# Optimization experiments

Measured on AMD Instinct MI355X. Metric: run time of the kernel, lower is better.

## Reference

```python
import jax, jax.numpy as jnp
import numpy as np
from jax import lax

EPS = 1e-5
T, N, E = 10, 10000, 320000
C_IN, C_HID, C_OUT = 16, 32, 16


def _stgcn_layer(x, edge_index, edge_weight, tw, tb, gw, gb, gamma, beta):
    # x: [T, N, Cin] -> temporal conv over T per node
    xc = jnp.transpose(x, (1, 2, 0))  # [N, Cin, T]
    y = lax.conv_general_dilated(xc, tw, window_strides=(1,), padding=((1, 1),),
                                 dimension_numbers=("NCH", "OIH", "NCH"))
    y = y + tb[None, :, None]
    y = jnp.clip(y, -10.0, 10.0)
    # InstanceNorm1d (affine, biased var over time axis)
    mu = jnp.mean(y, axis=-1, keepdims=True)
    var = jnp.mean((y - mu) ** 2, axis=-1, keepdims=True)
    y = (y - mu) * lax.rsqrt(var + EPS) * gamma[None, :, None] + beta[None, :, None]
    y = jax.nn.relu(y)
    h = jnp.transpose(y, (0, 2, 1))  # [N, T, C]

    n = h.shape[0]
    # GCNConv normalization (identical at every timestep -> computed once)
    ewn = jax.nn.softmax(edge_weight)  # softmax over all E edges
    loop = jnp.arange(n, dtype=edge_index.dtype)
    row = jnp.concatenate([edge_index[0], loop])  # sources (+self loops)
    col = jnp.concatenate([edge_index[1], loop])  # destinations
    w = jnp.concatenate([ewn, jnp.ones((n,), dtype=ewn.dtype)])
    deg = jax.ops.segment_sum(w, col, num_segments=n)
    dinv = jnp.where(deg > 0, lax.rsqrt(jnp.maximum(deg, EPS * 0 + 1e-30)), 0.0)
    norm = dinv[row] * w * dinv[col]  # [E+N]

    hw = jnp.einsum("ntc,cd->ntd", h, gw)  # [N, T, C]
    msg = hw[row] * norm[:, None, None]     # [E+N, T, C] gather
    agg = jax.ops.segment_sum(msg, col, num_segments=n) + gb  # scatter-add
    out = jnp.clip(jax.nn.relu(agg), -10.0, 10.0)
    return jnp.transpose(out, (1, 0, 2))  # [T, N, C]


def setup_inputs() -> dict:
    key = jax.random.key(0)
    ks = jax.random.split(key, 16)
    inp = {
        "x": jax.random.normal(ks[0], (T, N, C_IN), dtype=jnp.float32),
        "edge_index": jax.random.randint(ks[1], (2, E), 0, N, dtype=jnp.int32),
        "edge_weight": jax.random.uniform(ks[2], (E,), dtype=jnp.float32),
        # layer 1 (in -> hid)
        "l1_tw": jax.random.normal(ks[3], (C_HID, C_IN, 3), dtype=jnp.float32) * 0.02,
        "l1_tb": jnp.zeros((C_HID,), dtype=jnp.float32),
        "l1_gw": jax.random.normal(ks[4], (C_HID, C_HID), dtype=jnp.float32) * 0.1,
        "l1_gb": jnp.zeros((C_HID,), dtype=jnp.float32),
        "l1_gamma": jnp.ones((C_HID,), dtype=jnp.float32),
        "l1_beta": jnp.zeros((C_HID,), dtype=jnp.float32),
        # layer 2 (hid -> hid)
        "l2_tw": jax.random.normal(ks[5], (C_HID, C_HID, 3), dtype=jnp.float32) * 0.02,
        "l2_tb": jnp.zeros((C_HID,), dtype=jnp.float32),
        "l2_gw": jax.random.normal(ks[6], (C_HID, C_HID), dtype=jnp.float32) * 0.1,
        "l2_gb": jnp.zeros((C_HID,), dtype=jnp.float32),
        "l2_gamma": jnp.ones((C_HID,), dtype=jnp.float32),
        "l2_beta": jnp.zeros((C_HID,), dtype=jnp.float32),
        # output linear
        "out_w": jax.random.normal(ks[7], (C_HID, C_OUT), dtype=jnp.float32) * 0.1,
        "out_b": jnp.zeros((C_OUT,), dtype=jnp.float32),
    }
    return inp


def reference(x, edge_index, edge_weight,
              l1_tw, l1_tb, l1_gw, l1_gb, l1_gamma, l1_beta,
              l2_tw, l2_tb, l2_gw, l2_gb, l2_gamma, l2_beta,
              out_w, out_b):
    h = _stgcn_layer(x, edge_index, edge_weight, l1_tw, l1_tb, l1_gw, l1_gb, l1_gamma, l1_beta)
    h = _stgcn_layer(h, edge_index, edge_weight, l2_tw, l2_tb, l2_gw, l2_gb, l2_gamma, l2_beta)
    # per-timestep linear then mean over time == mean then linear, done faithfully
    outs = jnp.einsum("tnc,cd->tnd", h, out_w) + out_b
    return jnp.mean(outs, axis=0)  # [N, C_OUT]
```

## Files before the change

kernel.cpp:

```cpp
#include <hip/hip_runtime.h>
#include <hip/hip_bf16.h>
#include <string.h>


typedef __hip_bfloat16 bf16;

#define TSTEPS 10
#define TPAD 12
#define CHID 32
#define ROWELE (TSTEPS * CHID)
#define ROWW4 40

__device__ __forceinline__ float b2f(bf16 v) { return __bfloat162float(v); }
__device__ __forceinline__ float ldf(const void* p, long i, int bf) {
    return bf ? __bfloat162float(((const bf16*)p)[i]) : ((const float*)p)[i];
}
__device__ __forceinline__ int detect_bf(const unsigned* gbits) {
    return (gbits[0] != 0x3F800000u) ? 1 : 0;
}
__device__ __forceinline__ float bflo(unsigned u) { return __uint_as_float(u << 16); }
__device__ __forceinline__ float bfhi(unsigned u) { return __uint_as_float(u & 0xFFFF0000u); }
__device__ __forceinline__ unsigned pack2bf(float a, float b) {
    bf16 x = __float2bfloat16(a), y = __float2bfloat16(b);
    unsigned short ux, uy;
    memcpy(&ux, &x, 2); memcpy(&uy, &y, 2);
    return (unsigned)ux | ((unsigned)uy << 16);
}
__device__ __forceinline__ unsigned short bfbits(float a) {
    bf16 x = __float2bfloat16(a);
    unsigned short u; memcpy(&u, &x, 2);
    return u;
}
__device__ __forceinline__ void accum8(float* f, uint4 u, float w) {
    f[0] += w * bflo(u.x); f[1] += w * bfhi(u.x);
    f[2] += w * bflo(u.y); f[3] += w * bfhi(u.y);
    f[4] += w * bflo(u.z); f[5] += w * bfhi(u.z);
    f[6] += w * bflo(u.w); f[7] += w * bfhi(u.w);
}


__device__ __forceinline__ void edge_body(
    int bb, const void* __restrict__ ew, int bf, const int* __restrict__ ei,
    float* __restrict__ ewn, float* __restrict__ degx, int* __restrict__ cnt,
    float* __restrict__ sumexp, int E, int tid) {
    __shared__ float s_red[4];
    int i0 = (bb * 256 + tid) * 4;
    float e0 = 0.0f, e1 = 0.0f, e2 = 0.0f, e3 = 0.0f;
    if ((E & 3) == 0 && i0 + 3 < E) {
        float w0, w1, w2, w3;
        if (bf) {
            uint2 u = ((const uint2*)ew)[i0 >> 2];
            w0 = bflo(u.x); w1 = bfhi(u.x); w2 = bflo(u.y); w3 = bfhi(u.y);
        } else {
            float4 f = ((const float4*)ew)[i0 >> 2];
            w0 = f.x; w1 = f.y; w2 = f.z; w3 = f.w;
        }
        e0 = __expf(w0); e1 = __expf(w1); e2 = __expf(w2); e3 = __expf(w3);
        int4 c4 = *(const int4*)&ei[E + i0];
        atomicAdd(&degx[c4.x], e0); atomicAdd(&cnt[c4.x], 1);
        atomicAdd(&degx[c4.y], e1); atomicAdd(&cnt[c4.y], 1);
        atomicAdd(&degx[c4.z], e2); atomicAdd(&cnt[c4.z], 1);
        atomicAdd(&degx[c4.w], e3); atomicAdd(&cnt[c4.w], 1);
        *(float4*)&ewn[i0] = make_float4(e0, e1, e2, e3);
    } else {
        float es[4] = {0, 0, 0, 0};
        for (int j = 0; j < 4; j++) {
            int i = i0 + j;
            if (i < E) {
                float e = __expf(ldf(ew, i, bf));
                es[j] = e;
                ewn[i] = e;
                int c = ei[E + i];
                atomicAdd(&degx[c], e);
                atomicAdd(&cnt[c], 1);
            }
        }
        e0 = es[0]; e1 = es[1]; e2 = es[2]; e3 = es[3];
    }
    float v = (e0 + e1) + (e2 + e3);
    for (int o = 32; o > 0; o >>= 1) v += __shfl_down(v, o);
    int lane = tid & 63, wv = tid >> 6;
    if (lane == 0) s_red[wv] = v;
    __syncthreads();
    if (tid == 0) atomicAdd(sumexp, s_red[0] + s_red[1] + s_red[2] + s_red[3]);
}


template <int CIN, int LAYOUT>
__device__ __forceinline__ void conv_body(
    int bb, const void* __restrict__ in_, int bfw,
    const void* __restrict__ tw, const void* __restrict__ tb,
    const void* __restrict__ gamma, const void* __restrict__ beta,
    const void* __restrict__ gw,
    bf16* __restrict__ hw, int N, int tid) {
    constexpr int CO = CHID;
    __shared__ __align__(16) float s_in[8 * CIN * TPAD];
    __shared__ __align__(16) float s_h[8 * CO * TPAD];
    __shared__ __align__(16) unsigned s_tw01[CIN * CO];
    __shared__ __align__(16) unsigned short s_tw2[CIN * CO];
    __shared__ __align__(16) unsigned s_gwp[(CO / 2) * CO];

    int nl = tid >> 5, o = tid & 31;

    float tbv = ldf(tb, o, bfw);
    float gav = ldf(gamma, o, bfw);
    float bev = ldf(beta, o, bfw);

    for (int i = tid; i < CIN * CO; i += 256) {
        int ci = i / CO, oo = i % CO;
        long base = ((long)oo * CIN + ci) * 3;
        float w0 = ldf(tw, base, bfw);
        float w1 = ldf(tw, base + 1, bfw);
        float w2 = ldf(tw, base + 2, bfw);
        s_tw01[ci * CO + oo] = pack2bf(w0, w1);
        s_tw2[ci * CO + oo] = bfbits(w2);
    }
    for (int i = tid; i < (CO / 2) * CO; i += 256) {
        int cp = i / CO, oo = i % CO;
        s_gwp[i] = pack2bf(ldf(gw, (long)(2 * cp) * CO + oo, bfw),
                           ldf(gw, (long)(2 * cp + 1) * CO + oo, bfw));
    }

    int nb = bb * 8;

    if (LAYOUT == 0) {
        constexpr int CP = CIN / 2;
        for (int i2 = tid; i2 < 8 * TSTEPS * CP; i2 += 256) {
            int cp = i2 % CP;
            int t = (i2 / CP) % TSTEPS;
            int nn = i2 / (CP * TSTEPS);
            int n = nb + nn;
            float v0 = 0.0f, v1 = 0.0f;
            if (n < N) {
                long idx = (long)t * ((long)N * CIN) + (long)n * CIN + 2 * cp;
                if (bfw) {
                    unsigned u = ((const unsigned*)in_)[idx >> 1];
                    v0 = bflo(u); v1 = bfhi(u);
                } else {
                    float2 f = ((const float2*)in_)[idx >> 1];
                    v0 = f.x; v1 = f.y;
                }
            }
            int b = nn * (CIN * TPAD) + (2 * cp) * TPAD + t;
            s_in[b] = v0;
            s_in[b + TPAD] = v1;
        }
    } else {
        for (int i2 = tid; i2 < 8 * CIN * 5; i2 += 256) {
            int tp = i2 % 5;
            int ci = (i2 / 5) % CIN;
            int nn = i2 / (5 * CIN);
            int n = nb + nn;
            float v0 = 0.0f, v1 = 0.0f;
            if (n < N) {
                long idx = (long)n * (CIN * TSTEPS) + ci * TSTEPS + 2 * tp;
                unsigned u = ((const unsigned*)in_)[idx >> 1];
                v0 = bflo(u); v1 = bfhi(u);
            }
            int b = nn * (CIN * TPAD) + ci * TPAD + 2 * tp;
            s_in[b] = v0;
            s_in[b + 1] = v1;
        }
    }
    __syncthreads();

    int n = nb + nl;
    const float* xrow = &s_in[nl * CIN * TPAD];

    float acc[TSTEPS];
#pragma unroll
    for (int t = 0; t < TSTEPS; t++) acc[t] = tbv;

    for (int ci = 0; ci < CIN; ci++) {
        const float4* xp = (const float4*)&xrow[ci * TPAD];
        float4 A = xp[0], B = xp[1], C = xp[2];
        float xr[TSTEPS] = {A.x, A.y, A.z, A.w, B.x, B.y, B.z, B.w, C.x, C.y};
        unsigned w01 = s_tw01[ci * CO + o];
        float w0 = bflo(w01), w1 = bfhi(w01);
        float w2 = __uint_as_float(((unsigned)s_tw2[ci * CO + o]) << 16);
        acc[0] += xr[0] * w1 + xr[1] * w2;
#pragma unroll
        for (int t = 1; t < TSTEPS - 1; t++)
            acc[t] += xr[t - 1] * w0 + xr[t] * w1 + xr[t + 1] * w2;
        acc[TSTEPS - 1] += xr[TSTEPS - 2] * w0 + xr[TSTEPS - 1] * w1;
    }

#pragma unroll
    for (int t = 0; t < TSTEPS; t++) acc[t] = fminf(fmaxf(acc[t], -10.0f), 10.0f);
    float mu = 0.0f;
#pragma unroll
    for (int t = 0; t < TSTEPS; t++) mu += acc[t];
    mu *= 0.1f;
    float var = 0.0f;
#pragma unroll
    for (int t = 0; t < TSTEPS; t++) { float d = acc[t] - mu; var += d * d; }
    var *= 0.1f;
    float sc = gav * rsqrtf(var + 1e-5f);
    float h[TSTEPS];
#pragma unroll
    for (int t = 0; t < TSTEPS; t++) h[t] = fmaxf((acc[t] - mu) * sc + bev, 0.0f);

    float4* hp = (float4*)&s_h[nl * CO * TPAD + o * TPAD];
    hp[0] = make_float4(h[0], h[1], h[2], h[3]);
    hp[1] = make_float4(h[4], h[5], h[6], h[7]);
    hp[2] = make_float4(h[8], h[9], 0.0f, 0.0f);
    __syncthreads();

    float acc2[TSTEPS];
#pragma unroll
    for (int t = 0; t < TSTEPS; t++) acc2[t] = 0.0f;
    const float* hrow = &s_h[nl * CO * TPAD];
    for (int cp = 0; cp < CO / 2; cp++) {
        unsigned g2 = s_gwp[cp * CO + o];
        float g0 = bflo(g2), g1 = bfhi(g2);
        const float4* r0 = (const float4*)&hrow[(2 * cp) * TPAD];
        const float4* r1 = (const float4*)&hrow[(2 * cp + 1) * TPAD];
        float4 A0 = r0[0], B0 = r0[1], C0 = r0[2];
        float4 A1 = r1[0], B1 = r1[1], C1 = r1[2];
        acc2[0] += A0.x * g0 + A1.x * g1;
        acc2[1] += A0.y * g0 + A1.y * g1;
        acc2[2] += A0.z * g0 + A1.z * g1;
        acc2[3] += A0.w * g0 + A1.w * g1;
        acc2[4] += B0.x * g0 + B1.x * g1;
        acc2[5] += B0.y * g0 + B1.y * g1;
        acc2[6] += B0.z * g0 + B1.z * g1;
        acc2[7] += B0.w * g0 + B1.w * g1;
        acc2[8] += C0.x * g0 + C1.x * g1;
        acc2[9] += C0.y * g0 + C1.y * g1;
    }
    if (n < N) {
        unsigned* hwp = (unsigned*)hw;
        long base = (long)n * (ROWELE / 2) + o * (TSTEPS / 2);
#pragma unroll
        for (int j = 0; j < 5; j++)
            hwp[base + j] = pack2bf(acc2[2 * j], acc2[2 * j + 1]);
    }
}


__global__ __launch_bounds__(256) void edge_conv1_kernel(
    const void* __restrict__ ew, const unsigned* __restrict__ gbits,
    const int* __restrict__ ei,
    float* __restrict__ ewn, float* __restrict__ degx, int* __restrict__ cnt,
    float* __restrict__ sumexp, int E, int gE4,
    const void* __restrict__ x,
    const void* __restrict__ tw, const void* __restrict__ tb,
    const void* __restrict__ gamma, const void* __restrict__ beta,
    const void* __restrict__ gw,
    bf16* __restrict__ hw, int N) {
    int bf = detect_bf(gbits);
    int tid = threadIdx.x;
    if ((int)blockIdx.x < gE4) {
        edge_body(blockIdx.x, ew, bf, ei, ewn, degx, cnt, sumexp, E, tid);
    } else {
        conv_body<16, 0>(blockIdx.x - gE4, x, bf, tw, tb, gamma, beta, gw,
                         hw, N, tid);
    }
}

__global__ __launch_bounds__(256) void conv2_kernel(
    const void* __restrict__ in_, const unsigned* __restrict__ gbits,
    const void* __restrict__ tw, const void* __restrict__ tb,
    const void* __restrict__ gamma, const void* __restrict__ beta,
    const void* __restrict__ gw,
    bf16* __restrict__ hw, int N) {
    conv_body<32, 1>(blockIdx.x, in_, detect_bf(gbits), tw, tb, gamma, beta,
                     gw, hw, N, threadIdx.x);
}

__global__ __launch_bounds__(1024) void scan_kernel(const int* __restrict__ cnt,
                                                    const float* __restrict__ degx,
                                                    const float* __restrict__ sumexp,
                                                    float* __restrict__ dinv,
                                                    int* __restrict__ off, int N) {
    __shared__ int s[1024];
    int tid = threadIdx.x;
    float invS = 1.0f / (*sumexp);
    for (int i = tid; i < N; i += 1024) dinv[i] = rsqrtf(1.0f + degx[i] * invS);
    int chunk = (N + 1023) / 1024;
    int b0 = tid * chunk;
    int p = 0;
    for (int k = 0; k < chunk; k++) { int i = b0 + k; if (i < N) p += cnt[i]; }
    s[tid] = p;
    __syncthreads();
    for (int d = 1; d < 1024; d <<= 1) {
        int v = (tid >= d) ? s[tid - d] : 0;
        __syncthreads();
        s[tid] += v;
        __syncthreads();
    }
    int base = s[tid] - p;
    for (int k = 0; k < chunk; k++) {
        int i = b0 + k;
        if (i < N) {
            off[i] = base;
            base += cnt[i];
            if (i == N - 1) off[N] = base;
        }
    }
}


__global__ __launch_bounds__(256) void fill_kernel(const int* __restrict__ ei,
                                                   const float* __restrict__ ewn,
                                                   const float* __restrict__ dinv,
                                                   const float* __restrict__ sumexp,
                                                   const int* __restrict__ off,
                                                   int* __restrict__ cursor,
                                                   int2* __restrict__ csr, int E) {
    int i0 = (blockIdx.x * 256 + threadIdx.x) * 4;
    if (i0 >= E) return;
    float invS = 1.0f / (*sumexp);
    if ((E & 3) == 0 && i0 + 3 < E) {
        int4 r4 = *(const int4*)&ei[i0];
        int4 c4 = *(const int4*)&ei[E + i0];
        float4 e4 = *(const float4*)&ewn[i0];
        int rr[4] = {r4.x, r4.y, r4.z, r4.w};
        int cc[4] = {c4.x, c4.y, c4.z, c4.w};
        float ee[4] = {e4.x, e4.y, e4.z, e4.w};
#pragma unroll
        for (int j = 0; j < 4; j++) {
            int r = rr[j], c = cc[j];
            int p = atomicAdd(&cursor[c], 1);
            float w = dinv[r] * (ee[j] * invS) * dinv[c];
            csr[off[c] + p] = make_int2(r, __float_as_int(w));
        }
    } else {
        for (int j = 0; j < 4; j++) {
            int i = i0 + j;
            if (i >= E) break;
            int r = ei[i], c = ei[E + i];
            int p = atomicAdd(&cursor[c], 1);
            float w = dinv[r] * (ewn[i] * invS) * dinv[c];
            csr[off[c] + p] = make_int2(r, __float_as_int(w));
        }
    }
}


template <bool FINAL>
__global__ __launch_bounds__(320) void agg_kernel_t(
    const uint4* __restrict__ hw4, const int* __restrict__ off,
    const int2* __restrict__ csr,
    const float* __restrict__ dinv, const void* __restrict__ gb,
    const void* __restrict__ ow, const void* __restrict__ ob,
    const unsigned* __restrict__ gbits,
    void* __restrict__ out, int N) {
    __shared__ int2 s_sw[ROWELE];
    __shared__ float s_part[8 * ROWW4 * 9];
    __shared__ float s_hbar[CHID];
    __shared__ float s_ow[CHID * 16];
    __shared__ float s_ob[16];

    int bf = detect_bf(gbits);
    int n = blockIdx.x;
    int tid = threadIdx.x;
    int g = tid % ROWW4;
    int eo = tid / ROWW4;

    if (FINAL) {
        for (int i = tid; i < CHID * 16; i += ROWELE) s_ow[i] = ldf(ow, i, bf);
        if (tid < 16) s_ob[tid] = ldf(ob, tid, bf);
    }

    float facc[8];
#pragma unroll
    for (int j = 0; j < 8; j++) facc[j] = 0.0f;

    float dn = dinv[n];
    if (eo == 0) {
        uint4 u = hw4[n * ROWW4 + g];
        accum8(facc, u, dn * dn);
    }

    int beg = off[n], end = off[n + 1];
    for (int base = beg; base < end; base += ROWELE) {
        int m = min(ROWELE, end - base);
        if (tid < m) s_sw[tid] = csr[base + tid];
        __syncthreads();
        int kmax = (m + 7) >> 3;
        int k = 0;
        for (; k + 2 <= kmax; k += 2) {
            int j0 = (k << 3) + eo, j1 = j0 + 8;
            int c0 = min(j0, m - 1), c1 = min(j1, m - 1);
            int2 e0 = s_sw[c0], e1 = s_sw[c1];
            float w0 = (j0 < m) ? __int_as_float(e0.y) : 0.0f;
            float w1 = (j1 < m) ? __int_as_float(e1.y) : 0.0f;
            uint4 u0 = hw4[e0.x * ROWW4 + g];
            uint4 u1 = hw4[e1.x * ROWW4 + g];
            accum8(facc, u0, w0);
            accum8(facc, u1, w1);
        }
        if (k < kmax) {
            int j0 = (k << 3) + eo;
            int c0 = min(j0, m - 1);
            int2 e0 = s_sw[c0];
            float w0 = (j0 < m) ? __int_as_float(e0.y) : 0.0f;
            uint4 u0 = hw4[e0.x * ROWW4 + g];
            accum8(facc, u0, w0);
        }
        __syncthreads();
    }

    {
        float* rowp = &s_part[(eo * ROWW4 + g) * 9];
#pragma unroll
        for (int j = 0; j < 8; j++) rowp[j] = facc[j];
    }
    __syncthreads();
    int gg = tid >> 3, jj = tid & 7;
    float v = 0.0f;
#pragma unroll
    for (int s = 0; s < 8; s++) v += s_part[(s * ROWW4 + gg) * 9 + jj];
    int c = tid / TSTEPS;
    v += ldf(gb, c, bf);
    v = fminf(fmaxf(v, 0.0f), 10.0f);

    if (!FINAL) {
        ((bf16*)out)[(long)n * ROWELE + tid] = __float2bfloat16(v);
    } else {
        __syncthreads();
        s_part[tid] = v;
        __syncthreads();
        if (tid < CHID) {
            float s = 0.0f;
#pragma unroll
            for (int t = 0; t < TSTEPS; t++) s += s_part[tid * TSTEPS + t];
            s_hbar[tid] = s * 0.1f;
        }
        __syncthreads();
        if (tid < 16) {
            float a = s_ob[tid];
#pragma unroll
            for (int cc = 0; cc < CHID; cc++) a += s_hbar[cc] * s_ow[cc * 16 + tid];
            long oi = (long)n * 16 + tid;
            if (bf) ((bf16*)out)[oi] = __float2bfloat16(a);
            else    ((float*)out)[oi] = a;
        }
    }
}


extern "C" void kernel_launch(void* const* d_in, const int* in_sizes, int n_in,
                              void* d_out, int out_size, void* d_ws, size_t ws_size,
                              hipStream_t stream) {
    (void)n_in; (void)out_size; (void)ws_size;

    const void* x     = d_in[0];
    const int*  ei    = (const int*)d_in[1];
    const void* ew    = d_in[2];
    const void* l1_tw = d_in[3];
    const void* l1_tb = d_in[4];
    const void* l1_gw = d_in[5];
    const void* l1_gb = d_in[6];
    const unsigned* gbits = (const unsigned*)d_in[7];
    const void* l1_ga = d_in[7];
    const void* l1_be = d_in[8];
    const void* l2_tw = d_in[9];
    const void* l2_tb = d_in[10];
    const void* l2_gw = d_in[11];
    const void* l2_gb = d_in[12];
    const void* l2_ga = d_in[13];
    const void* l2_be = d_in[14];
    const void* out_w = d_in[15];
    const void* out_b = d_in[16];

    int N = in_sizes[0] / (TSTEPS * 16);
    int E = in_sizes[1] / 2;

    char* p = (char*)d_ws;
    auto alloc = [&](size_t bytes) -> char* {
        char* r = p;
        p += (bytes + 255) & ~(size_t)255;
        return r;
    };
    char* zbase   = p;
    float* sumexp = (float*)alloc(256);
    float* degx   = (float*)alloc((size_t)N * 4);
    int*   cnt    = (int*)alloc((size_t)N * 4);
    int*   cursor = (int*)alloc((size_t)N * 4);
    size_t zbytes = (size_t)(p - zbase);
    float* ewn     = (float*)alloc((size_t)E * 4);
    float* dinv    = (float*)alloc((size_t)N * 4);
    int*   offA    = (int*)alloc((size_t)(N + 1) * 4);
    int2*  csr     = (int2*)alloc((size_t)E * 8);
    bf16*  bufA    = (bf16*)alloc((size_t)N * ROWELE * 2);
    bf16*  bufB    = (bf16*)alloc((size_t)N * ROWELE * 2);

    int gE4 = (E + 1023) / 1024;
    int gConv = (N + 7) / 8;

    hipMemsetAsync(zbase, 0, zbytes, stream);
    hipLaunchKernelGGL(edge_conv1_kernel, dim3(gE4 + gConv), dim3(256), 0, stream,
                       ew, gbits, ei, ewn, degx, cnt, sumexp, E, gE4,
                       x, l1_tw, l1_tb, l1_ga, l1_be, l1_gw, bufA, N);
    hipLaunchKernelGGL(scan_kernel, dim3(1), dim3(1024), 0, stream,
                       cnt, degx, sumexp, dinv, offA, N);
    hipLaunchKernelGGL(fill_kernel, dim3(gE4), dim3(256), 0, stream,
                       ei, ewn, dinv, sumexp, offA, cursor, csr, E);

    hipLaunchKernelGGL((agg_kernel_t<false>), dim3(N), dim3(ROWELE), 0, stream,
                       (const uint4*)bufA, offA, csr, dinv, l1_gb,
                       nullptr, nullptr, gbits, (void*)bufB, N);
    hipLaunchKernelGGL(conv2_kernel, dim3(gConv), dim3(256), 0, stream,
                       (const void*)bufB, gbits, l2_tw, l2_tb, l2_ga, l2_be,
                       l2_gw, bufA, N);
    hipLaunchKernelGGL((agg_kernel_t<true>), dim3(N), dim3(ROWELE), 0, stream,
                       (const uint4*)bufA, offA, csr, dinv, l2_gb,
                       out_w, out_b, gbits, d_out, N);
}
```

Baseline: 279.7 us.

## Fuse edge, scan and CSR fill into one kernel with last-block grid sync

Merges the edge softmax/degree pass, the prefix scan and the CSR fill into a single launch alongside the first conv. The last edge block to finish, detected with an atomic counter, runs the scan with 256 threads and publishes a release flag, while the other edge blocks spin on that flag before filling. This removes two kernel launches and their inter-kernel gaps. It relies on all edge blocks being co-resident to avoid deadlock, the scan now runs on fewer threads, and spinning blocks occupy CU slots that conv blocks could use.

New measurement: 663.8 us. 2.37x slower.

```diff
diff --git a/kernel.cpp b/kernel.cpp
--- a/kernel.cpp
+++ b/kernel.cpp
@@ -83,6 +83,38 @@
     if (lane == 0) s_red[wv] = v;
     __syncthreads();
     if (tid == 0) atomicAdd(sumexp, s_red[0] + s_red[1] + s_red[2] + s_red[3]);
+}
+
+
+__device__ __forceinline__ void scan256(const int* __restrict__ cnt,
+                                        const float* __restrict__ degx,
+                                        const float* __restrict__ sumexp,
+                                        float* __restrict__ dinv,
+                                        int* __restrict__ off, int N, int tid) {
+    __shared__ int s_sc[256];
+    float invS = 1.0f / (*sumexp);
+    for (int i = tid; i < N; i += 256) dinv[i] = rsqrtf(1.0f + degx[i] * invS);
+    int chunk = (N + 255) / 256;
+    int b0 = tid * chunk;
+    int p = 0;
+    for (int k = 0; k < chunk; k++) { int i = b0 + k; if (i < N) p += cnt[i]; }
+    s_sc[tid] = p;
+    __syncthreads();
+    for (int d = 1; d < 256; d <<= 1) {
+        int v = (tid >= d) ? s_sc[tid - d] : 0;
+        __syncthreads();
+        s_sc[tid] += v;
+        __syncthreads();
+    }
+    int base = s_sc[tid] - p;
+    for (int k = 0; k < chunk; k++) {
+        int i = b0 + k;
+        if (i < N) {
+            off[i] = base;
+            base += cnt[i];
+            if (i == N - 1) off[N] = base;
+        }
+    }
 }
 
 
@@ -238,77 +270,12 @@
 }
 
 
-__global__ __launch_bounds__(256) void edge_conv1_kernel(
-    const void* __restrict__ ew, const unsigned* __restrict__ gbits,
-    const int* __restrict__ ei,
-    float* __restrict__ ewn, float* __restrict__ degx, int* __restrict__ cnt,
-    float* __restrict__ sumexp, int E, int gE4,
-    const void* __restrict__ x,
-    const void* __restrict__ tw, const void* __restrict__ tb,
-    const void* __restrict__ gamma, const void* __restrict__ beta,
-    const void* __restrict__ gw,
-    bf16* __restrict__ hw, int N) {
-    int bf = detect_bf(gbits);
-    int tid = threadIdx.x;
-    if ((int)blockIdx.x < gE4) {
-        edge_body(blockIdx.x, ew, bf, ei, ewn, degx, cnt, sumexp, E, tid);
-    } else {
-        conv_body<16, 0>(blockIdx.x - gE4, x, bf, tw, tb, gamma, beta, gw,
-                         hw, N, tid);
-    }
-}
-
-__global__ __launch_bounds__(256) void conv2_kernel(
-    const void* __restrict__ in_, const unsigned* __restrict__ gbits,
-    const void* __restrict__ tw, const void* __restrict__ tb,
-    const void* __restrict__ gamma, const void* __restrict__ beta,
-    const void* __restrict__ gw,
-    bf16* __restrict__ hw, int N) {
-    conv_body<32, 1>(blockIdx.x, in_, detect_bf(gbits), tw, tb, gamma, beta,
-                     gw, hw, N, threadIdx.x);
-}
-
-__global__ __launch_bounds__(1024) void scan_kernel(const int* __restrict__ cnt,
-                                                    const float* __restrict__ degx,
-                                                    const float* __restrict__ sumexp,
-                                                    float* __restrict__ dinv,
-                                                    int* __restrict__ off, int N) {
-    __shared__ int s[1024];
-    int tid = threadIdx.x;
-    float invS = 1.0f / (*sumexp);
-    for (int i = tid; i < N; i += 1024) dinv[i] = rsqrtf(1.0f + degx[i] * invS);
-    int chunk = (N + 1023) / 1024;
-    int b0 = tid * chunk;
-    int p = 0;
-    for (int k = 0; k < chunk; k++) { int i = b0 + k; if (i < N) p += cnt[i]; }
-    s[tid] = p;
-    __syncthreads();
-    for (int d = 1; d < 1024; d <<= 1) {
-        int v = (tid >= d) ? s[tid - d] : 0;
-        __syncthreads();
-        s[tid] += v;
-        __syncthreads();
-    }
-    int base = s[tid] - p;
-    for (int k = 0; k < chunk; k++) {
-        int i = b0 + k;
-        if (i < N) {
-            off[i] = base;
-            base += cnt[i];
-            if (i == N - 1) off[N] = base;
-        }
-    }
-}
-
-
-__global__ __launch_bounds__(256) void fill_kernel(const int* __restrict__ ei,
-                                                   const float* __restrict__ ewn,
-                                                   const float* __restrict__ dinv,
-                                                   const float* __restrict__ sumexp,
-                                                   const int* __restrict__ off,
-                                                   int* __restrict__ cursor,
-                                                   int2* __restrict__ csr, int E) {
-    int i0 = (blockIdx.x * 256 + threadIdx.x) * 4;
+__device__ __forceinline__ void fill_body(
+    int bb, const int* __restrict__ ei, const float* __restrict__ ewn,
+    const float* __restrict__ dinv, const float* __restrict__ sumexp,
+    const int* __restrict__ off, int* __restrict__ cursor,
+    int2* __restrict__ csr, int E, int tid) {
+    int i0 = (bb * 256 + tid) * 4;
     if (i0 >= E) return;
     float invS = 1.0f / (*sumexp);
     if ((E & 3) == 0 && i0 + 3 < E) {
@@ -335,6 +302,66 @@
             csr[off[c] + p] = make_int2(r, __float_as_int(w));
         }
     }
+}
+
+
+__global__ __launch_bounds__(256) void mega1_kernel(
+    const void* __restrict__ ew, const unsigned* __restrict__ gbits,
+    const int* __restrict__ ei,
+    float* __restrict__ ewn, float* __restrict__ degx, int* __restrict__ cnt,
+    float* __restrict__ sumexp, int E, int gE,
+    float* __restrict__ dinv, int* __restrict__ off, int* __restrict__ cursor,
+    int2* __restrict__ csr,
+    int* __restrict__ done, int* __restrict__ flag,
+    const void* __restrict__ x,
+    const void* __restrict__ tw, const void* __restrict__ tb,
+    const void* __restrict__ gamma, const void* __restrict__ beta,
+    const void* __restrict__ gw,
+    bf16* __restrict__ hw, int N) {
+    int tid = threadIdx.x;
+    int bf = detect_bf(gbits);
+    if ((int)blockIdx.x >= gE) {
+        conv_body<16, 0>(blockIdx.x - gE, x, bf, tw, tb, gamma, beta, gw,
+                         hw, N, tid);
+        return;
+    }
+    int bb = blockIdx.x;
+    edge_body(bb, ew, bf, ei, ewn, degx, cnt, sumexp, E, tid);
+
+    __shared__ int s_last;
+    __syncthreads();
+    if (tid == 0) {
+        __threadfence();
+        int prev = atomicAdd(done, 1);
+        s_last = (prev == gE - 1) ? 1 : 0;
+    }
+    __syncthreads();
+    if (s_last) {
+        scan256(cnt, degx, sumexp, dinv, off, N, tid);
+        __syncthreads();
+        if (tid == 0) {
+            __threadfence();
+            __hip_atomic_store(flag, 1, __ATOMIC_RELEASE, __HIP_MEMORY_SCOPE_AGENT);
+        }
+    } else {
+        if (tid == 0) {
+            while (__hip_atomic_load(flag, __ATOMIC_ACQUIRE,
+                                     __HIP_MEMORY_SCOPE_AGENT) == 0)
+                __builtin_amdgcn_s_sleep(8);
+        }
+        __syncthreads();
+    }
+    fill_body(bb, ei, ewn, dinv, sumexp, off, cursor, csr, E, tid);
+}
+
+__global__ __launch_bounds__(256) void conv2_kernel(
+    const void* __restrict__ in_, const unsigned* __restrict__ gbits,
+    const void* __restrict__ tw, const void* __restrict__ tb,
+    const void* __restrict__ gamma, const void* __restrict__ beta,
+    const void* __restrict__ gw,
+    bf16* __restrict__ hw, int N) {
+    conv_body<32, 1>(blockIdx.x, in_, detect_bf(gbits), tw, tb, gamma, beta,
+                     gw, hw, N, threadIdx.x);
 }
 
 
@@ -476,6 +503,8 @@
     };
     char* zbase   = p;
     float* sumexp = (float*)alloc(256);
+    int*   done   = (int*)alloc(256);
+    int*   flag   = (int*)alloc(256);
     float* degx   = (float*)alloc((size_t)N * 4);
     int*   cnt    = (int*)alloc((size_t)N * 4);
     int*   cursor = (int*)alloc((size_t)N * 4);
@@ -491,13 +520,10 @@
     int gConv = (N + 7) / 8;
 
     hipMemsetAsync(zbase, 0, zbytes, stream);
-    hipLaunchKernelGGL(edge_conv1_kernel, dim3(gE4 + gConv), dim3(256), 0, stream,
+    hipLaunchKernelGGL(mega1_kernel, dim3(gE4 + gConv), dim3(256), 0, stream,
                        ew, gbits, ei, ewn, degx, cnt, sumexp, E, gE4,
+                       dinv, offA, cursor, csr, done, flag,
                        x, l1_tw, l1_tb, l1_ga, l1_be, l1_gw, bufA, N);
-    hipLaunchKernelGGL(scan_kernel, dim3(1), dim3(1024), 0, stream,
-                       cnt, degx, sumexp, dinv, offA, N);
-    hipLaunchKernelGGL(fill_kernel, dim3(gE4), dim3(256), 0, stream,
-                       ei, ewn, dinv, sumexp, offA, cursor, csr, E);
 
     hipLaunchKernelGGL((agg_kernel_t<false>), dim3(N), dim3(ROWELE), 0, stream,
                        (const uint4*)bufA, offA, csr, dinv, l1_gb,
```
